# Optimization experiments

Hardware: AMD Instinct MI355X
Metric: run time of the kernel (lower is better)

## Reference

```python
import jax, jax.numpy as jnp
import numpy as np

EPS = 1e-6

def _ln(x, g, b):
    m = jnp.mean(x, axis=-1, keepdims=True)
    v = jnp.mean(jnp.square(x - m), axis=-1, keepdims=True)
    return (x - m) / jnp.sqrt(v + EPS) * g + b

def setup_inputs() -> dict:
    key = jax.random.key(0)
    ks = jax.random.split(key, 16)
    B, L, D = 4, 2048, 1024
    s = 0.02
    inp = {
        'q': jax.random.normal(ks[0], (B, L, D), jnp.float32),
        'k': jax.random.normal(ks[1], (B, L, D), jnp.float32),
        'v': jax.random.normal(ks[2], (B, L, D), jnp.float32),
    }
    wnames = ['Wq1', 'Wk1', 'Wv1', 'Wf1', 'Wq2', 'Wk2', 'Wv2', 'Wf2']
    for i, n in enumerate(wnames):
        inp[n] = jax.random.normal(ks[3 + i], (D, D), jnp.float32) * s
        inp['b' + n[1:]] = jnp.zeros((D,), jnp.float32)
    for n in ['q1', 'k1', 'v1', 'q2', 'k2', 'v2']:
        inp['g' + n] = jnp.ones((D,), jnp.float32)
        inp['B' + n] = jnp.zeros((D,), jnp.float32)
    return inp

def reference(q, k, v, Wq1, bq1, Wk1, bk1, Wv1, bv1, Wf1, bf1,
              Wq2, bq2, Wk2, bk2, Wv2, bv2, Wf2, bf2,
              gq1, Bq1, gk1, Bk1, gv1, Bv1, gq2, Bq2, gk2, Bk2, gv2, Bv2):
    # n_head = 1 (forced by LayerNorm(n_head*d_k) on last dim d_k); d_k = 1024
    temp = jnp.sqrt(jnp.asarray(q.shape[-1], q.dtype))

    def attn(qi, ki, vi):
        a = jax.nn.softmax(jnp.einsum('bqd,bkd->bqk', qi / temp, ki), axis=-1)
        return jnp.einsum('bqk,bkd->bqd', a, vi), a

    # layer 1
    q1 = q @ Wq1 + bq1
    k1 = k @ Wk1 + bk1
    v1 = v @ Wv1 + bv1
    residual1 = q1
    o1, _ = attn(_ln(q1, gq1, Bq1), _ln(k1, gk1, Bk1), _ln(v1, gv1, Bv1))
    o1 = o1 @ Wf1 + bf1
    # layer 2
    q2 = o1 @ Wq2 + bq2
    k2 = k @ Wk2 + bk2
    v2 = v @ Wv2 + bv2
    residual2 = q2
    o2, a2 = attn(_ln(q2, gq2, Bq2), _ln(k2, gk2, Bk2), _ln(v2, gv2, Bv2))
    out = o2 @ Wf2 + bf2
    # residuals in torch have shape (b, l, 1, d_k); cat on last dim -> (b, l, 1, 2*d_k)
    res = jnp.concatenate([residual1, residual2], axis=-1)[:, :, None, :]
    # attn2.squeeze() drops the singleton head dim -> (b, lq, lk)
    return out, res, a2
```

## Files before the change

kernel.cpp:

```cpp
#include <hip/hip_runtime.h>

#define DEV __device__ __forceinline__

using short8  = __attribute__((ext_vector_type(8))) short;
using floatx4 = __attribute__((ext_vector_type(4))) float;

DEV unsigned short f2bf(float f) {
  unsigned int u = __float_as_uint(f);
  u += 0x7FFFu + ((u >> 16) & 1u);
  return (unsigned short)(u >> 16);
}

DEV void stage16(void* lds, const void* g) {
#if defined(__has_builtin) && __has_builtin(__builtin_amdgcn_global_load_lds)
  __builtin_amdgcn_global_load_lds(
      (__attribute__((address_space(1))) void*)g,
      (__attribute__((address_space(3))) void*)lds, 16, 0, 0);
#else
  *(int4*)lds = *(const int4*)g;
#endif
}

DEV float wave_sum(float x) {
#pragma unroll
  for (int m = 32; m; m >>= 1) x += __shfl_xor(x, m);
  return x;
}
DEV float wave_max(float x) {
#pragma unroll
  for (int m = 32; m; m >>= 1) x = fmaxf(x, __shfl_xor(x, m));
  return x;
}

#define BM 128
#define BN 128
#define BK 32

__global__ __launch_bounds__(256)
void gemm_bt(const short* __restrict__ A, long long sAz,
             const short* __restrict__ Bt, long long sBz,
             const float* __restrict__ bias,
             float* __restrict__ Cf, long long sCfz,
             short* __restrict__ Cb, long long sCbz,
             float* __restrict__ C2, int offc2,
             int M, int N, int K) {
  const int z = blockIdx.z;
  A  += (long long)z * sAz;
  Bt += (long long)z * sBz;
  float* Cfz = Cf ? Cf + (long long)z * sCfz : (float*)0;
  short* Cbz = Cb ? Cb + (long long)z * sCbz : (short*)0;

  const int m0 = blockIdx.y * BM;
  const int n0 = blockIdx.x * BN;

  __shared__ __align__(16) short As[BM * BK];
  __shared__ __align__(16) short Bs[BN * BK];

  const int t    = threadIdx.x;
  const int lane = t & 63;
  const int w    = t >> 6;
  const int wr   = (w >> 1) * 64;
  const int wc   = (w & 1) * 64;
  const int mr   = lane & 15;
  const int kq   = lane >> 4;

  floatx4 acc[4][4];
#pragma unroll
  for (int i = 0; i < 4; ++i)
#pragma unroll
    for (int j = 0; j < 4; ++j)
      acc[i][j] = (floatx4){0.f, 0.f, 0.f, 0.f};

  for (int k0 = 0; k0 < K; k0 += BK) {
#pragma unroll
    for (int i = 0; i < 2; ++i) {
      const int c   = t + i * 256;
      const int row = c >> 2;
      const int cc  = c & 3;
      stage16(&As[c * 8], A  + (size_t)(m0 + row) * K + k0 + cc * 8);
      stage16(&Bs[c * 8], Bt + (size_t)(n0 + row) * K + k0 + cc * 8);
    }
    __syncthreads();

    short8 af[4], bf[4];
#pragma unroll
    for (int i = 0; i < 4; ++i)
      af[i] = *(const short8*)&As[(wr + i * 16 + mr) * BK + kq * 8];
#pragma unroll
    for (int j = 0; j < 4; ++j)
      bf[j] = *(const short8*)&Bs[(wc + j * 16 + mr) * BK + kq * 8];
#pragma unroll
    for (int i = 0; i < 4; ++i)
#pragma unroll
      for (int j = 0; j < 4; ++j)
        acc[i][j] = __builtin_amdgcn_mfma_f32_16x16x32_bf16(af[i], bf[j], acc[i][j], 0, 0, 0);
    __syncthreads();
  }

#pragma unroll
  for (int i = 0; i < 4; ++i) {
#pragma unroll
    for (int r = 0; r < 4; ++r) {
      const int row = m0 + wr + i * 16 + kq * 4 + r;
#pragma unroll
      for (int j = 0; j < 4; ++j) {
        const int col = n0 + wc + j * 16 + mr;
        float vv = acc[i][j][r];
        if (bias) vv += bias[col];
        if (Cfz) Cfz[(size_t)row * N + col] = vv;
        if (Cbz) Cbz[(size_t)row * N + col] = (short)f2bf(vv);
        if (C2)  C2[(size_t)row * 2048 + offc2 + col] = vv;
      }
    }
  }
}

__global__ __launch_bounds__(256)
void ln_kernel(const float* __restrict__ x, const float* __restrict__ gw,
               const float* __restrict__ bw, unsigned short* __restrict__ y,
               float scale) {
  const int row = blockIdx.x, t = threadIdx.x;
  const float4 v = ((const float4*)(x + (size_t)row * 1024))[t];
  float s  = v.x + v.y + v.z + v.w;
  float s2 = v.x * v.x + v.y * v.y + v.z * v.z + v.w * v.w;
  s = wave_sum(s);
  s2 = wave_sum(s2);
  __shared__ float r1[4], r2[4];
  const int w = t >> 6, lane = t & 63;
  if (!lane) { r1[w] = s; r2[w] = s2; }
  __syncthreads();
  s  = r1[0] + r1[1] + r1[2] + r1[3];
  s2 = r2[0] + r2[1] + r2[2] + r2[3];
  const float mean = s * (1.f / 1024.f);
  const float var  = s2 * (1.f / 1024.f) - mean * mean;
  const float rstd = 1.f / sqrtf(var + 1e-6f);
  const float4 g4 = ((const float4*)gw)[t];
  const float4 b4 = ((const float4*)bw)[t];
  ushort4 o;
  o.x = f2bf(((v.x - mean) * rstd * g4.x + b4.x) * scale);
  o.y = f2bf(((v.y - mean) * rstd * g4.y + b4.y) * scale);
  o.z = f2bf(((v.z - mean) * rstd * g4.z + b4.z) * scale);
  o.w = f2bf(((v.w - mean) * rstd * g4.w + b4.w) * scale);
  ((ushort4*)(y + (size_t)row * 1024))[t] = o;
}

__global__ __launch_bounds__(256)
void softmax_kernel(const float* __restrict__ S, unsigned short* __restrict__ P,
                    float* __restrict__ A2) {
  const int row = blockIdx.x, t = threadIdx.x;
  const float4* sr = (const float4*)(S + (size_t)row * 2048);
  float4 a = sr[t], b = sr[t + 256];
  float m = fmaxf(fmaxf(fmaxf(a.x, a.y), fmaxf(a.z, a.w)),
                  fmaxf(fmaxf(b.x, b.y), fmaxf(b.z, b.w)));
  m = wave_max(m);
  __shared__ float red[4];
  const int w = t >> 6, lane = t & 63;
  if (!lane) red[w] = m;
  __syncthreads();
  m = fmaxf(fmaxf(red[0], red[1]), fmaxf(red[2], red[3]));
  a.x = expf(a.x - m); a.y = expf(a.y - m); a.z = expf(a.z - m); a.w = expf(a.w - m);
  b.x = expf(b.x - m); b.y = expf(b.y - m); b.z = expf(b.z - m); b.w = expf(b.w - m);
  float s = a.x + a.y + a.z + a.w + b.x + b.y + b.z + b.w;
  s = wave_sum(s);
  __syncthreads();
  if (!lane) red[w] = s;
  __syncthreads();
  s = red[0] + red[1] + red[2] + red[3];
  const float inv = 1.f / s;
  a.x *= inv; a.y *= inv; a.z *= inv; a.w *= inv;
  b.x *= inv; b.y *= inv; b.z *= inv; b.w *= inv;
  ushort4 o0, o1;
  o0.x = f2bf(a.x); o0.y = f2bf(a.y); o0.z = f2bf(a.z); o0.w = f2bf(a.w);
  o1.x = f2bf(b.x); o1.y = f2bf(b.y); o1.z = f2bf(b.z); o1.w = f2bf(b.w);
  ((ushort4*)(P + (size_t)row * 2048))[t] = o0;
  ((ushort4*)(P + (size_t)row * 2048))[t + 256] = o1;
  if (A2) {
    float4* ar = (float4*)(A2 + (size_t)row * 2048);
    ar[t] = a;
    ar[t + 256] = b;
  }
}

__global__ __launch_bounds__(256)
void cast_kernel(const float* __restrict__ x, unsigned short* __restrict__ y, int n4) {
  const int i = blockIdx.x * 256 + threadIdx.x;
  if (i >= n4) return;
  const float4 v = ((const float4*)x)[i];
  ushort4 o;
  o.x = f2bf(v.x); o.y = f2bf(v.y); o.z = f2bf(v.z); o.w = f2bf(v.w);
  ((ushort4*)y)[i] = o;
}

__global__ __launch_bounds__(256)
void transpose_w_kernel(const float* __restrict__ in, unsigned short* __restrict__ out) {
  __shared__ unsigned short tile[64][65];
  const int tr0 = blockIdx.y * 64, tc0 = blockIdx.x * 64;
  const int x = threadIdx.x & 63, y = threadIdx.x >> 6;
#pragma unroll
  for (int i = 0; i < 16; ++i) {
    const int r = i * 4 + y;
    tile[r][x] = f2bf(in[(size_t)(tr0 + r) * 1024 + tc0 + x]);
  }
  __syncthreads();
#pragma unroll
  for (int i = 0; i < 16; ++i) {
    const int r = i * 4 + y;
    out[(size_t)(tc0 + r) * 1024 + tr0 + x] = tile[x][r];
  }
}

__global__ __launch_bounds__(256)
void transpose_v_kernel(const unsigned short* __restrict__ in, unsigned short* __restrict__ out) {
  __shared__ unsigned short tile[64][65];
  in  += (size_t)blockIdx.z * 2048 * 1024;
  out += (size_t)blockIdx.z * 1024 * 2048;
  const int tr0 = blockIdx.y * 64, tc0 = blockIdx.x * 64;
  const int x = threadIdx.x & 63, y = threadIdx.x >> 6;
#pragma unroll
  for (int i = 0; i < 16; ++i) {
    const int r = i * 4 + y;
    tile[r][x] = in[(size_t)(tr0 + r) * 1024 + tc0 + x];
  }
  __syncthreads();
#pragma unroll
  for (int i = 0; i < 16; ++i) {
    const int r = i * 4 + y;
    out[(size_t)(tc0 + r) * 2048 + tr0 + x] = tile[x][r];
  }
}

extern "C" void kernel_launch(void* const* d_in, const int* in_sizes, int n_in,
                              void* d_out, int out_size, void* d_ws, size_t ws_size,
                              hipStream_t stream) {
  const float* q = (const float*)d_in[0];
  const float* k = (const float*)d_in[1];
  const float* v = (const float*)d_in[2];
  const float* W[8];
  const float* bW[8];
  for (int i = 0; i < 8; ++i) {
    W[i]  = (const float*)d_in[3 + 2 * i];
    bW[i] = (const float*)d_in[4 + 2 * i];
  }
  const float* g_[6];
  const float* B_[6];
  for (int i = 0; i < 6; ++i) {
    g_[i] = (const float*)d_in[19 + 2 * i];
    B_[i] = (const float*)d_in[20 + 2 * i];
  }

  float* out_p = (float*)d_out;
  float* res_p = out_p + 8388608;
  float* a2_p  = res_p + 16777216;

  char* ws = (char*)d_ws;
  const size_t MBy = 1u << 20;
  unsigned short* WT   = (unsigned short*)ws;
  unsigned short* kb   = (unsigned short*)(ws + 16 * MBy);
  unsigned short* vb   = (unsigned short*)(ws + 32 * MBy);
  unsigned short* lnq  = (unsigned short*)(ws + 48 * MBy);
  unsigned short* lnk  = (unsigned short*)(ws + 64 * MBy);
  unsigned short* lnv  = (unsigned short*)(ws + 80 * MBy);
  unsigned short* lnvT = (unsigned short*)(ws + 96 * MBy);
  unsigned short* ofb  = (unsigned short*)(ws + 112 * MBy);
  unsigned short* ob   = (unsigned short*)(ws + 128 * MBy);
  float* Sbuf = (float*)(ws + 144 * MBy);
  float* qf   = (float*)(ws + 144 * MBy);
  float* kf   = (float*)(ws + 176 * MBy);
  float* vf   = (float*)(ws + 208 * MBy);
  unsigned short* P = (unsigned short*)(ws + 208 * MBy);

  const int n4 = 8192 * 1024 / 4;

  auto gemm = [&](const unsigned short* A, long long sAz,
                  const unsigned short* Bt, long long sBz, const float* bias,
                  float* Cf, long long sCfz, unsigned short* Cb, long long sCbz,
                  float* C2, int offc2, int M, int N, int K, int Z) {
    dim3 grid(N / 128, M / 128, Z);
    gemm_bt<<<grid, 256, 0, stream>>>((const short*)A, sAz, (const short*)Bt, sBz,
                                      bias, Cf, sCfz, (short*)Cb, sCbz, C2, offc2,
                                      M, N, K);
  };

  cast_kernel<<<n4 / 256, 256, 0, stream>>>(q, ob, n4);
  cast_kernel<<<n4 / 256, 256, 0, stream>>>(k, kb, n4);
  cast_kernel<<<n4 / 256, 256, 0, stream>>>(v, vb, n4);
  for (int i = 0; i < 8; ++i)
    transpose_w_kernel<<<dim3(16, 16), 256, 0, stream>>>(W[i], WT + (size_t)i * 1024 * 1024);

  gemm(ob, 0, WT + 0u * 1048576, 0, bW[0], qf, 0, 0, 0, res_p, 0,    8192, 1024, 1024, 1);
  gemm(kb, 0, WT + 1u * 1048576, 0, bW[1], kf, 0, 0, 0, 0, 0,        8192, 1024, 1024, 1);
  gemm(vb, 0, WT + 2u * 1048576, 0, bW[2], vf, 0, 0, 0, 0, 0,        8192, 1024, 1024, 1);
  ln_kernel<<<8192, 256, 0, stream>>>(qf, g_[0], B_[0], lnq, 1.f / 32.f);
  ln_kernel<<<8192, 256, 0, stream>>>(kf, g_[1], B_[1], lnk, 1.f);
  ln_kernel<<<8192, 256, 0, stream>>>(vf, g_[2], B_[2], lnv, 1.f);
  transpose_v_kernel<<<dim3(16, 32, 4), 256, 0, stream>>>(lnv, lnvT);
  gemm(lnq, 2048ll * 1024, lnk, 2048ll * 1024, 0, Sbuf, 2048ll * 2048, 0, 0, 0, 0,
       2048, 2048, 1024, 4);
  softmax_kernel<<<8192, 256, 0, stream>>>(Sbuf, P, (float*)0);
  gemm(P, 2048ll * 2048, lnvT, 1024ll * 2048, 0, 0, 0, ob, 2048ll * 1024, 0, 0,
       2048, 1024, 2048, 4);
  gemm(ob, 0, WT + 3u * 1048576, 0, bW[3], 0, 0, ofb, 0, 0, 0, 8192, 1024, 1024, 1);

  gemm(ofb, 0, WT + 4u * 1048576, 0, bW[4], qf, 0, 0, 0, res_p, 1024, 8192, 1024, 1024, 1);
  gemm(kb, 0, WT + 5u * 1048576, 0, bW[5], kf, 0, 0, 0, 0, 0,         8192, 1024, 1024, 1);
  gemm(vb, 0, WT + 6u * 1048576, 0, bW[6], vf, 0, 0, 0, 0, 0,         8192, 1024, 1024, 1);
  ln_kernel<<<8192, 256, 0, stream>>>(qf, g_[3], B_[3], lnq, 1.f / 32.f);
  ln_kernel<<<8192, 256, 0, stream>>>(kf, g_[4], B_[4], lnk, 1.f);
  ln_kernel<<<8192, 256, 0, stream>>>(vf, g_[5], B_[5], lnv, 1.f);
  transpose_v_kernel<<<dim3(16, 32, 4), 256, 0, stream>>>(lnv, lnvT);
  gemm(lnq, 2048ll * 1024, lnk, 2048ll * 1024, 0, Sbuf, 2048ll * 2048, 0, 0, 0, 0,
       2048, 2048, 1024, 4);
  softmax_kernel<<<8192, 256, 0, stream>>>(Sbuf, P, a2_p);
  gemm(P, 2048ll * 2048, lnvT, 1024ll * 2048, 0, 0, 0, ob, 2048ll * 1024, 0, 0,
       2048, 1024, 2048, 4);
  gemm(ob, 0, WT + 7u * 1048576, 0, bW[7], out_p, 0, 0, 0, 0, 0, 8192, 1024, 1024, 1);
}
```

Measured before the change: 1.063 ms.

## Batch layer-2 K/V projections with layer 1 and merge small launches

Weights Wk1/Wk2 and Wv1/Wv2 are laid out adjacently so the K and V projections for both layers run as a single N=2048 GEMM each, with bias moved into the LayerNorm. The five independent LayerNorms, the three casts, the eight weight transposes and both V transposes are each merged into one multi-job launch. This cuts kernel launch count and lets the small kernels fill the GPU better, at the cost of a larger workspace and strided fp32 intermediates.

```diff
diff --git a/kernel.cpp b/kernel.cpp
--- a/kernel.cpp
+++ b/kernel.cpp
@@ -115,12 +115,29 @@
   }
 }
 
-__global__ __launch_bounds__(256)
-void ln_kernel(const float* __restrict__ x, const float* __restrict__ gw,
-               const float* __restrict__ bw, unsigned short* __restrict__ y,
-               float scale) {
+struct LnJob {
+  const float* x;
+  const float* bias;
+  const float* g;
+  const float* Bb;
+  unsigned short* y;
+  int ldx;
+  float scale;
+};
+
+__global__ __launch_bounds__(256)
+void ln_multi(LnJob j0, LnJob j1, LnJob j2, LnJob j3, LnJob j4) {
+  LnJob jb = j0;
+  if (blockIdx.y == 1) jb = j1;
+  else if (blockIdx.y == 2) jb = j2;
+  else if (blockIdx.y == 3) jb = j3;
+  else if (blockIdx.y == 4) jb = j4;
   const int row = blockIdx.x, t = threadIdx.x;
-  const float4 v = ((const float4*)(x + (size_t)row * 1024))[t];
+  float4 v = ((const float4*)(jb.x + (size_t)row * jb.ldx))[t];
+  if (jb.bias) {
+    const float4 b4 = ((const float4*)jb.bias)[t];
+    v.x += b4.x; v.y += b4.y; v.z += b4.z; v.w += b4.w;
+  }
   float s  = v.x + v.y + v.z + v.w;
   float s2 = v.x * v.x + v.y * v.y + v.z * v.z + v.w * v.w;
   s = wave_sum(s);
@@ -134,14 +151,14 @@
   const float mean = s * (1.f / 1024.f);
   const float var  = s2 * (1.f / 1024.f) - mean * mean;
   const float rstd = 1.f / sqrtf(var + 1e-6f);
-  const float4 g4 = ((const float4*)gw)[t];
-  const float4 b4 = ((const float4*)bw)[t];
+  const float4 g4 = ((const float4*)jb.g)[t];
+  const float4 b4 = ((const float4*)jb.Bb)[t];
   ushort4 o;
-  o.x = f2bf(((v.x - mean) * rstd * g4.x + b4.x) * scale);
-  o.y = f2bf(((v.y - mean) * rstd * g4.y + b4.y) * scale);
-  o.z = f2bf(((v.z - mean) * rstd * g4.z + b4.z) * scale);
-  o.w = f2bf(((v.w - mean) * rstd * g4.w + b4.w) * scale);
-  ((ushort4*)(y + (size_t)row * 1024))[t] = o;
+  o.x = f2bf(((v.x - mean) * rstd * g4.x + b4.x) * jb.scale);
+  o.y = f2bf(((v.y - mean) * rstd * g4.y + b4.y) * jb.scale);
+  o.z = f2bf(((v.z - mean) * rstd * g4.z + b4.z) * jb.scale);
+  o.w = f2bf(((v.w - mean) * rstd * g4.w + b4.w) * jb.scale);
+  ((ushort4*)(jb.y + (size_t)row * 1024))[t] = o;
 }
 
 __global__ __launch_bounds__(256)
@@ -182,18 +199,28 @@
 }
 
 __global__ __launch_bounds__(256)
-void cast_kernel(const float* __restrict__ x, unsigned short* __restrict__ y, int n4) {
+void cast3_kernel(const float* __restrict__ x0, const float* __restrict__ x1,
+                  const float* __restrict__ x2, unsigned short* __restrict__ y0,
+                  unsigned short* __restrict__ y1, unsigned short* __restrict__ y2) {
+  const float* x = blockIdx.y == 0 ? x0 : (blockIdx.y == 1 ? x1 : x2);
+  unsigned short* y = blockIdx.y == 0 ? y0 : (blockIdx.y == 1 ? y1 : y2);
   const int i = blockIdx.x * 256 + threadIdx.x;
-  if (i >= n4) return;
   const float4 v = ((const float4*)x)[i];
   ushort4 o;
   o.x = f2bf(v.x); o.y = f2bf(v.y); o.z = f2bf(v.z); o.w = f2bf(v.w);
   ((ushort4*)y)[i] = o;
 }
 
-__global__ __launch_bounds__(256)
-void transpose_w_kernel(const float* __restrict__ in, unsigned short* __restrict__ out) {
+struct W8 {
+  const float* src[8];
+  unsigned short* dst[8];
+};
+
+__global__ __launch_bounds__(256)
+void transpose_w8_kernel(W8 p) {
   __shared__ unsigned short tile[64][65];
+  const float* in = p.src[blockIdx.z];
+  unsigned short* out = p.dst[blockIdx.z];
   const int tr0 = blockIdx.y * 64, tc0 = blockIdx.x * 64;
   const int x = threadIdx.x & 63, y = threadIdx.x >> 6;
 #pragma unroll
@@ -210,10 +237,14 @@
 }
 
 __global__ __launch_bounds__(256)
-void transpose_v_kernel(const unsigned short* __restrict__ in, unsigned short* __restrict__ out) {
+void transpose_v8_kernel(const unsigned short* __restrict__ in0,
+                         const unsigned short* __restrict__ in1,
+                         unsigned short* __restrict__ out0,
+                         unsigned short* __restrict__ out1) {
   __shared__ unsigned short tile[64][65];
-  in  += (size_t)blockIdx.z * 2048 * 1024;
-  out += (size_t)blockIdx.z * 1024 * 2048;
+  const int zz = blockIdx.z & 3;
+  const unsigned short* in = (blockIdx.z < 4 ? in0 : in1) + (size_t)zz * 2048 * 1024;
+  unsigned short* out = (blockIdx.z < 4 ? out0 : out1) + (size_t)zz * 1024 * 2048;
   const int tr0 = blockIdx.y * 64, tc0 = blockIdx.x * 64;
   const int x = threadIdx.x & 63, y = threadIdx.x >> 6;
 #pragma unroll
@@ -254,22 +285,29 @@
 
   char* ws = (char*)d_ws;
   const size_t MBy = 1u << 20;
-  unsigned short* WT   = (unsigned short*)ws;
-  unsigned short* kb   = (unsigned short*)(ws + 16 * MBy);
-  unsigned short* vb   = (unsigned short*)(ws + 32 * MBy);
-  unsigned short* lnq  = (unsigned short*)(ws + 48 * MBy);
-  unsigned short* lnk  = (unsigned short*)(ws + 64 * MBy);
-  unsigned short* lnv  = (unsigned short*)(ws + 80 * MBy);
-  unsigned short* lnvT = (unsigned short*)(ws + 96 * MBy);
-  unsigned short* ofb  = (unsigned short*)(ws + 112 * MBy);
-  unsigned short* ob   = (unsigned short*)(ws + 128 * MBy);
-  float* Sbuf = (float*)(ws + 144 * MBy);
-  float* qf   = (float*)(ws + 144 * MBy);
-  float* kf   = (float*)(ws + 176 * MBy);
-  float* vf   = (float*)(ws + 208 * MBy);
-  unsigned short* P = (unsigned short*)(ws + 208 * MBy);
-
-  const int n4 = 8192 * 1024 / 4;
+  unsigned short* WqT1  = (unsigned short*)(ws + 0 * MBy);
+  unsigned short* WfT1  = (unsigned short*)(ws + 2 * MBy);
+  unsigned short* WqT2  = (unsigned short*)(ws + 4 * MBy);
+  unsigned short* WfT2  = (unsigned short*)(ws + 6 * MBy);
+  unsigned short* WkT12 = (unsigned short*)(ws + 8 * MBy);
+  unsigned short* WvT12 = (unsigned short*)(ws + 12 * MBy);
+  unsigned short* qb    = (unsigned short*)(ws + 16 * MBy);
+  unsigned short* kb    = (unsigned short*)(ws + 32 * MBy);
+  unsigned short* vb    = (unsigned short*)(ws + 48 * MBy);
+  float* kf   = (float*)(ws + 64 * MBy);
+  float* vf   = (float*)(ws + 128 * MBy);
+  float* Sbuf = (float*)(ws + 64 * MBy);
+  unsigned short* P = (unsigned short*)(ws + 128 * MBy);
+  float* qf   = (float*)(ws + 192 * MBy);
+  unsigned short* lnq   = (unsigned short*)(ws + 224 * MBy);
+  unsigned short* lnk1  = (unsigned short*)(ws + 240 * MBy);
+  unsigned short* lnk2  = (unsigned short*)(ws + 256 * MBy);
+  unsigned short* lnv1  = (unsigned short*)(ws + 272 * MBy);
+  unsigned short* lnv2  = (unsigned short*)(ws + 288 * MBy);
+  unsigned short* lnvT1 = (unsigned short*)(ws + 304 * MBy);
+  unsigned short* lnvT2 = (unsigned short*)(ws + 320 * MBy);
+  unsigned short* ofb   = (unsigned short*)(ws + 336 * MBy);
+  unsigned short* ob    = (unsigned short*)(ws + 352 * MBy);
 
   auto gemm = [&](const unsigned short* A, long long sAz,
                   const unsigned short* Bt, long long sBz, const float* bias,
@@ -280,38 +318,50 @@
                                       bias, Cf, sCfz, (short*)Cb, sCbz, C2, offc2,
                                       M, N, K);
   };
-
-  cast_kernel<<<n4 / 256, 256, 0, stream>>>(q, ob, n4);
-  cast_kernel<<<n4 / 256, 256, 0, stream>>>(k, kb, n4);
-  cast_kernel<<<n4 / 256, 256, 0, stream>>>(v, vb, n4);
-  for (int i = 0; i < 8; ++i)
-    transpose_w_kernel<<<dim3(16, 16), 256, 0, stream>>>(W[i], WT + (size_t)i * 1024 * 1024);
-
-  gemm(ob, 0, WT + 0u * 1048576, 0, bW[0], qf, 0, 0, 0, res_p, 0,    8192, 1024, 1024, 1);
-  gemm(kb, 0, WT + 1u * 1048576, 0, bW[1], kf, 0, 0, 0, 0, 0,        8192, 1024, 1024, 1);
-  gemm(vb, 0, WT + 2u * 1048576, 0, bW[2], vf, 0, 0, 0, 0, 0,        8192, 1024, 1024, 1);
-  ln_kernel<<<8192, 256, 0, stream>>>(qf, g_[0], B_[0], lnq, 1.f / 32.f);
-  ln_kernel<<<8192, 256, 0, stream>>>(kf, g_[1], B_[1], lnk, 1.f);
-  ln_kernel<<<8192, 256, 0, stream>>>(vf, g_[2], B_[2], lnv, 1.f);
-  transpose_v_kernel<<<dim3(16, 32, 4), 256, 0, stream>>>(lnv, lnvT);
-  gemm(lnq, 2048ll * 1024, lnk, 2048ll * 1024, 0, Sbuf, 2048ll * 2048, 0, 0, 0, 0,
+  LnJob nil{};
+
+  cast3_kernel<<<dim3(8192, 3), 256, 0, stream>>>(q, k, v, qb, kb, vb);
+  W8 w8;
+  w8.src[0] = W[0]; w8.dst[0] = WqT1;
+  w8.src[1] = W[1]; w8.dst[1] = WkT12;
+  w8.src[2] = W[2]; w8.dst[2] = WvT12;
+  w8.src[3] = W[3]; w8.dst[3] = WfT1;
+  w8.src[4] = W[4]; w8.dst[4] = WqT2;
+  w8.src[5] = W[5]; w8.dst[5] = WkT12 + 1024 * 1024;
+  w8.src[6] = W[6]; w8.dst[6] = WvT12 + 1024 * 1024;
+  w8.src[7] = W[7]; w8.dst[7] = WfT2;
+  transpose_w8_kernel<<<dim3(16, 16, 8), 256, 0, stream>>>(w8);
+
+  gemm(kb, 8192ll * 1024, WkT12, 2048ll * 1024, 0, kf, 8192ll * 2048, 0, 0, 0, 0,
+       8192, 2048, 1024, 2);
+  gemm(qb, 0, WqT1, 0, bW[0], qf, 0, 0, 0, res_p, 0, 8192, 1024, 1024, 1);
+
+  {
+    LnJob jk1{kf,        bW[1], g_[1], B_[1], lnk1, 2048, 1.f};
+    LnJob jk2{kf + 1024, bW[5], g_[4], B_[4], lnk2, 2048, 1.f};
+    LnJob jv1{vf,        bW[2], g_[2], B_[2], lnv1, 2048, 1.f};
+    LnJob jv2{vf + 1024, bW[6], g_[5], B_[5], lnv2, 2048, 1.f};
+    LnJob jq1{qf,        0,     g_[0], B_[0], lnq,  1024, 1.f / 32.f};
+    ln_multi<<<dim3(8192, 5), 256, 0, stream>>>(jk1, jk2, jv1, jv2, jq1);
+  }
+  transpose_v8_kernel<<<dim3(16, 32, 8), 256, 0, stream>>>(lnv1, lnv2, lnvT1, lnvT2);
+
+  gemm(lnq, 2048ll * 1024, lnk1, 2048ll * 1024, 0, Sbuf, 2048ll * 2048, 0, 0, 0, 0,
        2048, 2048, 1024, 4);
   softmax_kernel<<<8192, 256, 0, stream>>>(Sbuf, P, (float*)0);
-  gemm(P, 2048ll * 2048, lnvT, 1024ll * 2048, 0, 0, 0, ob, 2048ll * 1024, 0, 0,
+  gemm(P, 2048ll * 2048, lnvT1, 1024ll * 2048, 0, 0, 0, ob, 2048ll * 1024, 0, 0,
        2048, 1024, 2048, 4);
-  gemm(ob, 0, WT + 3u * 1048576, 0, bW[3], 0, 0, ofb, 0, 0, 0, 8192, 1024, 1024, 1);
-
-  gemm(ofb, 0, WT + 4u * 1048576, 0, bW[4], qf, 0, 0, 0, res_p, 1024, 8192, 1024, 1024, 1);
-  gemm(kb, 0, WT + 5u * 1048576, 0, bW[5], kf, 0, 0, 0, 0, 0,         8192, 1024, 1024, 1);
-  gemm(vb, 0, WT + 6u * 1048576, 0, bW[6], vf, 0, 0, 0, 0, 0,         8192, 1024, 1024, 1);
-  ln_kernel<<<8192, 256, 0, stream>>>(qf, g_[3], B_[3], lnq, 1.f / 32.f);
-  ln_kernel<<<8192, 256, 0, stream>>>(kf, g_[4], B_[4], lnk, 1.f);
-  ln_kernel<<<8192, 256, 0, stream>>>(vf, g_[5], B_[5], lnv, 1.f);
-  transpose_v_kernel<<<dim3(16, 32, 4), 256, 0, stream>>>(lnv, lnvT);
-  gemm(lnq, 2048ll * 1024, lnk, 2048ll * 1024, 0, Sbuf, 2048ll * 2048, 0, 0, 0, 0,
+  gemm(ob, 0, WfT1, 0, bW[3], 0, 0, ofb, 0, 0, 0, 8192, 1024, 1024, 1);
+
+  gemm(ofb, 0, WqT2, 0, bW[4], qf, 0, 0, 0, res_p, 1024, 8192, 1024, 1024, 1);
+  {
+    LnJob jq2{qf, 0, g_[3], B_[3], lnq, 1024, 1.f / 32.f};
+    ln_multi<<<dim3(8192, 1), 256, 0, stream>>>(jq2, nil, nil, nil, nil);
+  }
+  gemm(lnq, 2048ll * 1024, lnk2, 2048ll * 1024, 0, Sbuf, 2048ll * 2048, 0, 0, 0, 0,
        2048, 2048, 1024, 4);
   softmax_kernel<<<8192, 256, 0, stream>>>(Sbuf, P, a2_p);
-  gemm(P, 2048ll * 2048, lnvT, 1024ll * 2048, 0, 0, 0, ob, 2048ll * 1024, 0, 0,
+  gemm(P, 2048ll * 2048, lnvT2, 1024ll * 2048, 0, 0, 0, ob, 2048ll * 1024, 0, 0,
        2048, 1024, 2048, 4);
-  gemm(ob, 0, WT + 7u * 1048576, 0, bW[7], out_p, 0, 0, 0, 0, 0, 8192, 1024, 1024, 1);
-}
+  gemm(ob, 0, WfT2, 0, bW[7], out_p, 0, 0, 0, 0, 0, 8192, 1024, 1024, 1);
+}
```

New measurement: 1.004 ms. 5.6% less time.
